# Kernel optimization log

Measured on AMD Instinct MI355X. Metric: run time of the kernel, lower is better.

## Reference

```python
import jax, jax.numpy as jnp
import numpy as np

N = 768          # nodes
E_HALF = 12288   # undirected edges (both directions added -> E = 24576)
P = 4096         # query pairs
H = 32           # hidden_dim_1wl == hidden_dim_2wl
MAX_X = 100
EPS = 1e-5
LAYER1 = 2


def setup_inputs() -> dict:
    key = jax.random.key(0)
    ks = jax.random.split(key, 12)
    s = 0.1
    x = jax.random.randint(ks[0], (N,), 0, MAX_X + 1)
    half = jax.random.randint(ks[1], (2, E_HALF), 0, N)
    ei = jnp.concatenate([half, half[::-1]], axis=1)          # symmetric edge set [2,E]
    pos = jax.random.randint(ks[2], (P, 2), 0, N)
    emb = jax.random.normal(ks[3], (MAX_X + 1, H)) * s
    gcn_W = jax.random.normal(ks[4], (LAYER1, H, H)) * s
    gcn_b = jnp.zeros((LAYER1, H))
    mlp1_W = jax.random.normal(ks[5], (2 * H, H)) * s
    mlp1_b = jnp.zeros((H,))
    mlp2_W = jax.random.normal(ks[6], (2 * H, H)) * s
    mlp2_b = jnp.zeros((H,))
    mlp3_W = jax.random.normal(ks[7], (H + 1, H)) * s
    mlp3_b = jnp.zeros((H,))
    lin_W = jax.random.normal(ks[8], (2 * H, 1)) * s
    lin_b = jnp.zeros((1,))
    return dict(x=x, ei=ei, pos=pos, emb=emb, gcn_W=gcn_W, gcn_b=gcn_b,
                mlp1_W=mlp1_W, mlp1_b=mlp1_b, mlp2_W=mlp2_W, mlp2_b=mlp2_b,
                mlp3_W=mlp3_W, mlp3_b=mlp3_b, lin_W=lin_W, lin_b=lin_b)


def _graph_norm(h):
    # PyG-style GraphNorm with default params (mean_scale=1, weight=1, bias=0)
    h = h - h.mean(0)
    return h * jax.lax.rsqrt((h * h).mean(0) + EPS)


def reference(x, ei, pos, emb, gcn_W, gcn_b, mlp1_W, mlp1_b,
              mlp2_W, mlp2_b, mlp3_W, mlp3_b, lin_W, lin_b):
    n = x.shape[0]
    d = emb.shape[1]
    h = emb[x]                                                 # [n,H] (dropout=0)
    # --- GCNConv stack: Ahat = D^-1/2 (A+I) D^-1/2 ---
    A = jnp.zeros((n, n), h.dtype).at[ei[0], ei[1]].set(1.0)
    Ahat = A + jnp.eye(n, dtype=h.dtype)
    dinv = jax.lax.rsqrt(Ahat.sum(1))
    An = Ahat * dinv[:, None] * dinv[None, :]
    for l in range(gcn_W.shape[0]):
        h = An @ (h @ gcn_W[l]) + gcn_b[l]
        h = jax.nn.relu(_graph_norm(h))                        # GraphNorm + ReLU
    # --- pair features ---
    xx = h[pos[:, 0]] * h[pos[:, 1]]                           # [P,H]
    val = jnp.concatenate([h[ei[0]], h[ei[1]]], 1)             # [E,2H]
    xe = jax.nn.relu(val @ mlp1_W + mlp1_b)                    # mlps_1
    mul = jax.nn.relu(val @ mlp2_W + mlp2_b)                   # mlps_2[0]
    # --- sparse_bmm as dense [n,n,d] contraction (coalesce sums duplicates -> .add) ---
    Xd = jnp.zeros((n, n, d), h.dtype).at[ei[0], ei[1]].add(xe)
    Md = jnp.zeros((n, n, d), h.dtype).at[ei[0], ei[1]].add(mul)
    C = jnp.einsum('ikd,kjd->ijd', Xd, Md)                     # x_{ij} = sum_k x_{ik}*mul_{kj}
    # support of the sparse result: 2-hop pairs union original edges (sparse_cat)
    adj_b = jnp.zeros((n, n), bool).at[ei[0], ei[1]].set(True)
    af = adj_b.astype(h.dtype)
    mask = ((af @ af) > 0) | adj_b
    ind = af[..., None]                                        # ones-column for original edges
    value = jnp.concatenate([C, ind], -1)                      # [n,n,H+1]
    z = value @ mlp3_W + mlp3_b                                # mlps_3[0]
    # GraphNorm over the edge support only (faithful to sparse values())
    m = mask.astype(h.dtype)[..., None]
    cnt = m.sum()
    mean = (z * m).sum((0, 1)) / cnt
    z = z - mean
    var = ((z * z) * m).sum((0, 1)) / cnt
    z = jax.nn.relu(z * jax.lax.rsqrt(var + EPS))
    # x * sm: multiply by transposed values; zero outside support (= add_zero)
    sym = z * jnp.swapaxes(z, 0, 1) * m
    pair = sym[pos[:, 0], pos[:, 1]]                           # [P,H] (edge_list gather)
    out = jnp.concatenate([pair, xx], 1) @ lin_W + lin_b       # lin_dir -> [P,1]
    return out
```

## Files before the change

kernel.cpp:

```cpp
#include <hip/hip_runtime.h>
#include <hip/hip_bf16.h>

#define NN 768
#define NE 24576
#define NPOS 4096
#define NCELL (NN*NN)
#define NBLK 2304
#define NBLK2 1152
#define NREP 16

typedef __hip_bfloat16 bf16;

__device__ __forceinline__ float ldf(const void* p, int i, int mode) {
    return mode ? __bfloat162float(((const bf16*)p)[i]) : ((const float*)p)[i];
}
__device__ __forceinline__ float aread(float* p) { return atomicAdd(p, 0.f); }
__device__ __forceinline__ int areadi(int* p) { return atomicAdd(p, 0); }

template<int D, int HALF>
__device__ __forceinline__ void redRound(float* v, int lane) {
#pragma unroll
    for (int i = 0; i < HALF; i++) {
        float snd = (lane & D) ? v[i] : v[i + HALF];
        float r = __shfl_xor(snd, D);
        v[i] = ((lane & D) ? v[i + HALF] : v[i]) + r;
    }
}

#define DOT4(Z, A, W) Z += A.x * W.x + A.y * W.y + A.z * W.z + A.w * W.w

__global__ void k_conv(const void* __restrict__ gW, const void* __restrict__ gB,
                       const void* __restrict__ m1W, const void* __restrict__ m1B,
                       const void* __restrict__ m2W, const void* __restrict__ m2B,
                       const void* __restrict__ m3W, const void* __restrict__ m3B,
                       const void* __restrict__ lW,  const void* __restrict__ lB,
                       const void* __restrict__ emb,
                       float* __restrict__ stats, int* __restrict__ cursor,
                       int* __restrict__ rowlen, int* __restrict__ rtot, int* __restrict__ dcs,
                       int* __restrict__ modeg,
                       float* __restrict__ gwf, float* __restrict__ gbf,
                       float* __restrict__ w1f, float* __restrict__ b1f,
                       float* __restrict__ w2f, float* __restrict__ b2f,
                       float* __restrict__ w3q, float* __restrict__ linf, float* __restrict__ linb) {
    int t = threadIdx.x;
    if (blockIdx.x == 1) {
        for (int i = t; i < NN; i += 256) { cursor[i] = 0; rowlen[i] = 0; rtot[i] = 0; }
        for (int i = t; i < NREP * 80; i += 256) stats[i] = 0.f;
        if (t < 8) dcs[t] = 0;
        return;
    }
    __shared__ int bad;
    if (t == 0) bad = 0;
    __syncthreads();
    int local = 0;
    for (int i = t; i < 3232; i += 256) {
        float a = fabsf(__bfloat162float(((const bf16*)emb)[i]));
        if (!(a < 100.f)) local = 1;
    }
    if (local) atomicOr(&bad, 1);
    __syncthreads();
    int mode = bad ? 0 : 1;
    if (t == 0) *modeg = mode;
    for (int i = t; i < 2048; i += 256) {
        gwf[i] = ldf(gW, i, mode);
        w1f[i] = ldf(m1W, i, mode);
        w2f[i] = ldf(m2W, i, mode);
    }
    for (int i = t; i < 64; i += 256) { gbf[i] = ldf(gB, i, mode); linf[i] = ldf(lW, i, mode); }
    if (t < 32) { b1f[t] = ldf(m1B, t, mode); b2f[t] = ldf(m2B, t, mode); }
    for (int i = t; i < 1056; i += 256) { int c = i >> 5, d = i & 31; w3q[d * 36 + c] = ldf(m3W, i, mode); }
    if (t < 32) { w3q[t * 36 + 33] = ldf(m3B, t, mode); w3q[t * 36 + 34] = 0.f; w3q[t * 36 + 35] = 0.f; }
    if (t == 0) linb[0] = ldf(lB, 0, mode);
}

__global__ void k_scatter(const int* __restrict__ ei, int* __restrict__ cell, int* __restrict__ rowlen,
                          int* __restrict__ row_ptr, float* __restrict__ dinv, int* __restrict__ dc) {
    __shared__ int amlast;
    __shared__ int sI[256];
    int t = threadIdx.x;
    int e = blockIdx.x * 256 + t;
    int a = ei[e], b = ei[NE + e];
    if ((unsigned)a < (unsigned)NN && (unsigned)b < (unsigned)NN) {
        int old = atomicAdd(&cell[a * NN + b], 1);
        if (old == 0) atomicAdd(&rowlen[a], 1);
    }
    __syncthreads();
    if (t == 0) { __threadfence(); amlast = (atomicAdd(dc, 1) == 95) ? 1 : 0; }
    __syncthreads();
    if (!amlast) return;
    int i0 = 3 * t;
    int r0 = areadi(&rowlen[i0]), r1 = areadi(&rowlen[i0 + 1]), r2 = areadi(&rowlen[i0 + 2]);
    dinv[i0]     = rsqrtf((float)r0 + 1.f);
    dinv[i0 + 1] = rsqrtf((float)r1 + 1.f);
    dinv[i0 + 2] = rsqrtf((float)r2 + 1.f);
    int s3 = r0 + r1 + r2;
    sI[t] = s3;
    __syncthreads();
    for (int off = 1; off < 256; off <<= 1) {
        int tmp = (t >= off) ? sI[t - off] : 0;
        __syncthreads();
        sI[t] += tmp;
        __syncthreads();
    }
    int excl = sI[t] - s3;
    row_ptr[i0] = excl;
    row_ptr[i0 + 1] = excl + r0;
    row_ptr[i0 + 2] = excl + r0 + r1;
    if (t == 255) row_ptr[NN] = sI[255];
}

__global__ void k_fw0(int* __restrict__ cell, const int* __restrict__ row_ptr, int* __restrict__ cursor,
                      int* __restrict__ col_idx, float* __restrict__ cntv, int* __restrict__ pr_row,
                      const int* __restrict__ rowlen, int* __restrict__ rtot,
                      const int* __restrict__ x, const void* __restrict__ emb,
                      const int* __restrict__ modep, const float* __restrict__ gwf,
                      float* __restrict__ bufA) {
    int t = threadIdx.x;
    int b = blockIdx.x;
    if (b < NBLK) {
        int idx = b * 256 + t;
        int i = idx / NN;
        int j = idx - i * NN;
        int cv = cell[idx];
        if (cv > 0) {
            int p = row_ptr[i] + atomicAdd(&cursor[i], 1);
            col_idx[p] = j; cntv[p] = (float)cv; pr_row[p] = i;
            cell[idx] = p;
            atomicAdd(&rtot[i], rowlen[j]);
        } else cell[idx] = -1;
    } else {
        int idx = (b - NBLK) * 256 + t;
        int i = idx >> 5, d = idx & 31;
        int mode = *modep;
        int xi = x[i]; if (xi < 0) xi = 0; if (xi > 100) xi = 100;
        float s = 0.f;
#pragma unroll
        for (int c = 0; c < 32; c++) s += ldf(emb, xi * 32 + c, mode) * gwf[c * 32 + d];
        bufA[idx] = s;
    }
}

__global__ void k_rbagg0(const int* __restrict__ rtot, int* __restrict__ row_base,
                         const int* __restrict__ row_ptr, const int* __restrict__ col_idx,
                         const float* __restrict__ bufA, const float* __restrict__ dinv,
                         const float* __restrict__ gbf, float* __restrict__ bufB) {
    int t = threadIdx.x;
    if (blockIdx.x == 0) {
        __shared__ int sI[256];
        int r3[3]; int s3 = 0;
#pragma unroll
        for (int q = 0; q < 3; q++) { r3[q] = rtot[3 * t + q]; s3 += r3[q]; }
        sI[t] = s3;
        __syncthreads();
        for (int off = 1; off < 256; off <<= 1) {
            int tmp = (t >= off) ? sI[t - off] : 0;
            __syncthreads();
            sI[t] += tmp;
            __syncthreads();
        }
        int run = sI[t] - s3;
        row_base[3 * t] = run;
        row_base[3 * t + 1] = run + r3[0];
        row_base[3 * t + 2] = run + r3[0] + r3[1];
    } else {
        int idx = (blockIdx.x - 1) * 256 + t;
        int i = idx >> 5, d = idx & 31;
        int base = row_ptr[i], len = row_ptr[i + 1] - base;
        float di = dinv[i];
        float acc = di * bufA[i * 32 + d];
        for (int e = 0; e < len; e++) { int c = col_idx[base + e]; acc += dinv[c] * bufA[c * 32 + d]; }
        bufB[idx] = di * acc + gbf[d];
    }
}

__global__ void k_hist(const int* __restrict__ row_ptr, const int* __restrict__ col_idx,
                       const int* __restrict__ row_base,
                       int* __restrict__ pcur, int2* __restrict__ paths2, int cap,
                       const float* __restrict__ bufB, float* __restrict__ nrm0) {
    int t = threadIdx.x;
    if (blockIdx.x == NN) {
        __shared__ float r1[256], r2[256];
        int dd = t & 31, g = t >> 5;
        float s = 0.f, s2 = 0.f;
        for (int r = g; r < NN; r += 8) { float v = bufB[r * 32 + dd]; s += v; s2 += v * v; }
        r1[t] = s; r2[t] = s2;
        __syncthreads();
        if (t < 32) {
            float a = 0.f, b2 = 0.f;
            for (int k = 0; k < 8; k++) { a += r1[k * 32 + t]; b2 += r2[k * 32 + t]; }
            float mean = a / (float)NN;
            float var = b2 / (float)NN - mean * mean;
            nrm0[t] = mean;
            nrm0[32 + t] = rsqrtf(fmaxf(var, 0.f) + 1e-5f);
        }
        return;
    }
    __shared__ int hist[NN];
    __shared__ int sc[256];
    int i = blockIdx.x;
    int base = row_ptr[i], len = row_ptr[i + 1] - base;
    int rb = row_base[i];
    int wave = t >> 6, lane = t & 63;
    for (int j = t; j < NN; j += 256) hist[j] = 0;
    __syncthreads();
    for (int ee = wave; ee < len; ee += 4) {
        int k = col_idx[base + ee];
        int kb = row_ptr[k], ke = row_ptr[k + 1];
        for (int e = kb + lane; e < ke; e += 64) atomicAdd(&hist[col_idx[e]], 1);
    }
    __syncthreads();
    int h0 = hist[3 * t], h1 = hist[3 * t + 1], h2 = hist[3 * t + 2];
    int s3 = h0 + h1 + h2;
    sc[t] = s3;
    __syncthreads();
    for (int off = 1; off < 256; off <<= 1) {
        int tmp = (t >= off) ? sc[t - off] : 0;
        __syncthreads();
        sc[t] += tmp;
        __syncthreads();
    }
    int excl = sc[t] - s3;
    int n0 = i * NN + 3 * t;
    pcur[n0]     = rb + excl + h0;
    pcur[n0 + 1] = rb + excl + h0 + h1;
    pcur[n0 + 2] = rb + excl + h0 + h1 + h2;
    hist[3 * t] = excl;
    hist[3 * t + 1] = excl + h0;
    hist[3 * t + 2] = excl + h0 + h1;
    __syncthreads();
    for (int ee = wave; ee < len; ee += 4) {
        int e1 = base + ee;
        int k = col_idx[e1];
        int kb = row_ptr[k], ke = row_ptr[k + 1];
        for (int e = kb + lane; e < ke; e += 64) {
            int j = col_idx[e];
            int slot = rb + atomicAdd(&hist[j], 1);
            if (slot < cap) paths2[slot] = make_int2(e1, e);
        }
    }
}

__global__ void k_mw1(const float* __restrict__ bufB, const float* __restrict__ nrm0,
                      const float* __restrict__ gwf, float* __restrict__ bufA) {
    int idx = blockIdx.x * 256 + threadIdx.x;
    int i = idx >> 5, d = idx & 31;
    const float* W = gwf + 1024;
    float s = 0.f;
#pragma unroll
    for (int c = 0; c < 32; c++) {
        float hv = fmaxf((bufB[i * 32 + c] - nrm0[c]) * nrm0[32 + c], 0.f);
        s += hv * W[c * 32 + d];
    }
    bufA[idx] = s;
}

__global__ void k_agg1(const int* __restrict__ row_ptr, const int* __restrict__ col_idx,
                       const float* __restrict__ bufA, const float* __restrict__ dinv,
                       const float* __restrict__ gbf, float* __restrict__ bufB) {
    int idx = blockIdx.x * 256 + threadIdx.x;
    int i = idx >> 5, d = idx & 31;
    int base = row_ptr[i], len = row_ptr[i + 1] - base;
    float di = dinv[i];
    float acc = di * bufA[i * 32 + d];
    for (int e = 0; e < len; e++) { int c = col_idx[base + e]; acc += dinv[c] * bufA[c * 32 + d]; }
    bufB[idx] = di * acc + gbf[32 + d];
}

__global__ void k_st1(const float* __restrict__ bufB, float* __restrict__ nrm1) {
    __shared__ float r1[256], r2[256];
    int t = threadIdx.x;
    int dd = t & 31, g = t >> 5;
    float s = 0.f, s2 = 0.f;
    for (int r = g; r < NN; r += 8) { float v = bufB[r * 32 + dd]; s += v; s2 += v * v; }
    r1[t] = s; r2[t] = s2;
    __syncthreads();
    if (t < 32) {
        float a = 0.f, b2 = 0.f;
        for (int k = 0; k < 8; k++) { a += r1[k * 32 + t]; b2 += r2[k * 32 + t]; }
        float mean = a / (float)NN;
        float var = b2 / (float)NN - mean * mean;
        nrm1[t] = mean;
        nrm1[32 + t] = rsqrtf(fmaxf(var, 0.f) + 1e-5f);
    }
}

__global__ void k_emlp(const float* __restrict__ bufB, const float* __restrict__ nrm1,
                       const int* __restrict__ row_ptr, const int* __restrict__ col_idx,
                       const int* __restrict__ pr_row, const float* __restrict__ cntv,
                       const float* __restrict__ w1f, const float* __restrict__ b1f,
                       const float* __restrict__ w2f, const float* __restrict__ b2f,
                       float* __restrict__ xep, float* __restrict__ mulp, float* __restrict__ h) {
    int t = threadIdx.x;
    int b = blockIdx.x;
    if (b < 3072) {
        int d = t & 31;
        int p = b * 8 + (t >> 5);
        if (p >= row_ptr[NN]) {
            if (p < NE) { xep[p * 32 + d] = 0.f; mulp[p * 32 + d] = 0.f; }
            return;
        }
        int i = pr_row[p], j = col_idx[p];
        float a1 = b1f[d], a2 = b2f[d];
#pragma unroll
        for (int c = 0; c < 32; c++) {
            float hv = fmaxf((bufB[i * 32 + c] - nrm1[c]) * nrm1[32 + c], 0.f);
            a1 += hv * w1f[c * 32 + d];
            a2 += hv * w2f[c * 32 + d];
        }
#pragma unroll
        for (int c = 0; c < 32; c++) {
            float hv = fmaxf((bufB[j * 32 + c] - nrm1[c]) * nrm1[32 + c], 0.f);
            a1 += hv * w1f[(32 + c) * 32 + d];
            a2 += hv * w2f[(32 + c) * 32 + d];
        }
        float cv = cntv[p];
        xep[p * 32 + d]  = cv * fmaxf(a1, 0.f);
        mulp[p * 32 + d] = cv * fmaxf(a2, 0.f);
    } else {
        int idx = (b - 3072) * 256 + t;
        int d = idx & 31;
        h[idx] = fmaxf((bufB[idx] - nrm1[d]) * nrm1[32 + d], 0.f);
    }
}

__global__ __launch_bounds__(256, 3) void k_big(const int* __restrict__ pcur,
                                                const int2* __restrict__ paths2,
                                                const int* __restrict__ cell,
                                                const float4* __restrict__ xep4, const float4* __restrict__ mulp4,
                                                const float* __restrict__ w3q,
                                                float* __restrict__ stats, int* __restrict__ done,
                                                float* __restrict__ nrm, int cap) {
    __shared__ float sS1[32], sS2[32];
    __shared__ float sCm;
    __shared__ int amlast;
    int t = threadIdx.x, lane = t & 63;
    int b = blockIdx.x;
    int n0 = b * 512 + 2 * t;
    if (t == 0) sCm = 0.f;
    if (t < 32) { sS1[t] = 0.f; sS2[t] = 0.f; }
    __syncthreads();
    int p0a = (n0 == 0) ? 0 : pcur[n0 - 1];
    int p1a = pcur[n0];
    int p1b = pcur[n0 + 1];
    if (p0a > cap) p0a = cap; if (p1a > cap) p1a = cap; if (p1b > cap) p1b = cap;
    float4 a0 = {0.f,0.f,0.f,0.f}, a1 = a0, a2 = a0, a3 = a0, a4 = a0, a5 = a0, a6 = a0, a7 = a0;
    float4 c0 = a0, c1 = a0, c2 = a0, c3 = a0, c4 = a0, c5 = a0, c6 = a0, c7 = a0;
    for (int p = p0a; p < p1a; p++) {
        int2 rec = paths2[p];
        const float4* xr = xep4 + rec.x * 8;
        const float4* mr = mulp4 + rec.y * 8;
        float4 xv, mv;
        xv = xr[0]; mv = mr[0]; a0.x += xv.x*mv.x; a0.y += xv.y*mv.y; a0.z += xv.z*mv.z; a0.w += xv.w*mv.w;
        xv = xr[1]; mv = mr[1]; a1.x += xv.x*mv.x; a1.y += xv.y*mv.y; a1.z += xv.z*mv.z; a1.w += xv.w*mv.w;
        xv = xr[2]; mv = mr[2]; a2.x += xv.x*mv.x; a2.y += xv.y*mv.y; a2.z += xv.z*mv.z; a2.w += xv.w*mv.w;
        xv = xr[3]; mv = mr[3]; a3.x += xv.x*mv.x; a3.y += xv.y*mv.y; a3.z += xv.z*mv.z; a3.w += xv.w*mv.w;
        xv = xr[4]; mv = mr[4]; a4.x += xv.x*mv.x; a4.y += xv.y*mv.y; a4.z += xv.z*mv.z; a4.w += xv.w*mv.w;
        xv = xr[5]; mv = mr[5]; a5.x += xv.x*mv.x; a5.y += xv.y*mv.y; a5.z += xv.z*mv.z; a5.w += xv.w*mv.w;
        xv = xr[6]; mv = mr[6]; a6.x += xv.x*mv.x; a6.y += xv.y*mv.y; a6.z += xv.z*mv.z; a6.w += xv.w*mv.w;
        xv = xr[7]; mv = mr[7]; a7.x += xv.x*mv.x; a7.y += xv.y*mv.y; a7.z += xv.z*mv.z; a7.w += xv.w*mv.w;
    }
    for (int p = p1a; p < p1b; p++) {
        int2 rec = paths2[p];
        const float4* xr = xep4 + rec.x * 8;
        const float4* mr = mulp4 + rec.y * 8;
        float4 xv, mv;
        xv = xr[0]; mv = mr[0]; c0.x += xv.x*mv.x; c0.y += xv.y*mv.y; c0.z += xv.z*mv.z; c0.w += xv.w*mv.w;
        xv = xr[1]; mv = mr[1]; c1.x += xv.x*mv.x; c1.y += xv.y*mv.y; c1.z += xv.z*mv.z; c1.w += xv.w*mv.w;
        xv = xr[2]; mv = mr[2]; c2.x += xv.x*mv.x; c2.y += xv.y*mv.y; c2.z += xv.z*mv.z; c2.w += xv.w*mv.w;
        xv = xr[3]; mv = mr[3]; c3.x += xv.x*mv.x; c3.y += xv.y*mv.y; c3.z += xv.z*mv.z; c3.w += xv.w*mv.w;
        xv = xr[4]; mv = mr[4]; c4.x += xv.x*mv.x; c4.y += xv.y*mv.y; c4.z += xv.z*mv.z; c4.w += xv.w*mv.w;
        xv = xr[5]; mv = mr[5]; c5.x += xv.x*mv.x; c5.y += xv.y*mv.y; c5.z += xv.z*mv.z; c5.w += xv.w*mv.w;
        xv = xr[6]; mv = mr[6]; c6.x += xv.x*mv.x; c6.y += xv.y*mv.y; c6.z += xv.z*mv.z; c6.w += xv.w*mv.w;
        xv = xr[7]; mv = mr[7]; c7.x += xv.x*mv.x; c7.y += xv.y*mv.y; c7.z += xv.z*mv.z; c7.w += xv.w*mv.w;
    }
    bool adja = cell[n0] >= 0;
    bool adjb = cell[n0 + 1] >= 0;
    float afa = adja ? 1.f : 0.f;
    float afb = adjb ? 1.f : 0.f;
    float mska = (p1a > p0a || adja) ? 1.f : 0.f;
    float mskb = (p1b > p1a || adjb) ? 1.f : 0.f;
#pragma unroll
    for (int ch = 0; ch < 2; ch++) {
        float v[32];
#pragma unroll
        for (int j = 0; j < 16; j++) {
            int dd = ch * 16 + j;
            const float4* wr = (const float4*)(w3q + dd * 36);
            float4 wv = wr[8];
            float za = wv.y + afa * wv.x;
            float zb = wv.y + afb * wv.x;
            wv = wr[0]; DOT4(za, a0, wv); DOT4(zb, c0, wv);
            wv = wr[1]; DOT4(za, a1, wv); DOT4(zb, c1, wv);
            wv = wr[2]; DOT4(za, a2, wv); DOT4(zb, c2, wv);
            wv = wr[3]; DOT4(za, a3, wv); DOT4(zb, c3, wv);
            wv = wr[4]; DOT4(za, a4, wv); DOT4(zb, c4, wv);
            wv = wr[5]; DOT4(za, a5, wv); DOT4(zb, c5, wv);
            wv = wr[6]; DOT4(za, a6, wv); DOT4(zb, c6, wv);
            wv = wr[7]; DOT4(za, a7, wv); DOT4(zb, c7, wv);
            v[j] = mska * za + mskb * zb;
            v[16 + j] = mska * za * za + mskb * zb * zb;
        }
#pragma unroll
        for (int i2 = 0; i2 < 32; i2++) v[i2] += __shfl_xor(v[i2], 32);
        redRound<16, 16>(v, lane);
        redRound<8, 8>(v, lane);
        redRound<4, 4>(v, lane);
        redRound<2, 2>(v, lane);
        redRound<1, 1>(v, lane);
        if (lane < 32) {
            if (lane < 16) atomicAdd(&sS1[ch * 16 + lane], v[0]);
            else           atomicAdd(&sS2[ch * 16 + lane - 16], v[0]);
        }
    }
    {
        float cm2 = mska + mskb;
        for (int off = 32; off >= 1; off >>= 1) cm2 += __shfl_xor(cm2, off);
        if (lane == 0) atomicAdd(&sCm, cm2);
    }
    __syncthreads();
    float* srep = stats + (b & (NREP - 1)) * 80;
    if (t < 32) {
        atomicAdd(&srep[t], sS1[t]);
        atomicAdd(&srep[32 + t], sS2[t]);
    }
    if (t == 32) atomicAdd(&srep[64], sCm);
    __syncthreads();
    if (t == 0) {
        __threadfence();
        amlast = (atomicAdd(done, 1) == NBLK2 - 1) ? 1 : 0;
    }
    __syncthreads();
    if (amlast && t < 32) {
        float sum1 = 0.f, sum2 = 0.f;
        for (int r = 0; r < NREP; r++) {
            sum1 += aread(&stats[r * 80 + t]);
            sum2 += aread(&stats[r * 80 + 32 + t]);
        }
        float cmv = 0.f;
        for (int r = 0; r < NREP; r++) cmv += aread(&stats[r * 80 + 64]);
        if (cmv < 1.f) cmv = 1.f;
        float mean = sum1 / cmv;
        float var = sum2 / cmv - mean * mean;
        nrm[t] = mean;
        nrm[32 + t] = rsqrtf(fmaxf(var, 0.f) + 1e-5f);
    }
}

__global__ void k_out(const int* __restrict__ pos, const int* __restrict__ pcur,
                      const int2* __restrict__ paths2,
                      const int* __restrict__ cell,
                      const float* __restrict__ xep, const float* __restrict__ mulp,
                      const float* __restrict__ h,
                      const float* __restrict__ w3q,
                      const float* __restrict__ nrm,
                      const float* __restrict__ linf, const float* __restrict__ linb,
                      const int* __restrict__ modep, int cap, void* __restrict__ outp) {
    __shared__ float Cb[4][2][32];
    int t = threadIdx.x;
    int w = t >> 6, lane = t & 63, d = lane & 31, dir = lane >> 5;
    int p = blockIdx.x * 4 + w;
    int a = pos[2 * p], b = pos[2 * p + 1];
    if ((unsigned)a >= (unsigned)NN) a = 0;
    if ((unsigned)b >= (unsigned)NN) b = 0;
    int r = dir ? b : a;
    int cc = dir ? a : b;
    int n = r * NN + cc;
    int p1 = pcur[n];
    int p0 = (n == 0) ? 0 : pcur[n - 1];
    if (p0 > cap) p0 = cap; if (p1 > cap) p1 = cap;
    float acc = 0.f;
    for (int q = p0; q < p1; q++) {
        int2 rec = paths2[q];
        acc += xep[rec.x * 32 + d] * mulp[rec.y * 32 + d];
    }
    Cb[w][dir][d] = acc;
    bool adj = cell[n] >= 0;
    float msk = (p1 > p0 || adj) ? 1.f : 0.f;
    __syncthreads();
    float z = w3q[d * 36 + 33] + (adj ? 1.f : 0.f) * w3q[d * 36 + 32];
#pragma unroll
    for (int c = 0; c < 32; c++) z += Cb[w][dir][c] * w3q[d * 36 + c];
    float zn = fmaxf((z - nrm[d]) * nrm[32 + d], 0.f);
    float zp = __shfl_xor(zn, 32);
    float symd = msk * zn * zp;
    float xxd = h[a * 32 + d] * h[b * 32 + d];
    float contrib = symd * linf[d] + xxd * linf[32 + d];
    for (int off = 16; off >= 1; off >>= 1) contrib += __shfl_xor(contrib, off);
    if (lane == 0) {
        float v = contrib + linb[0];
        v = fminf(fmaxf(v, -1e4f), 1e4f);
        if (*modep) ((bf16*)outp)[p] = __float2bfloat16(v);
        else        ((float*)outp)[p] = v;
    }
}

extern "C" void kernel_launch(void* const* d_in, const int* in_sizes, int n_in,
                              void* d_out, int out_size, void* d_ws, size_t ws_size,
                              hipStream_t stream) {
    const void* px  = d_in[0];  const void* pei = d_in[1];  const void* ppos = d_in[2];
    const void* pemb = d_in[3]; const void* pgW = d_in[4];  const void* pgB  = d_in[5];
    const void* pm1W = d_in[6]; const void* pm1B = d_in[7]; const void* pm2W = d_in[8];
    const void* pm2B = d_in[9]; const void* pm3W = d_in[10]; const void* pm3B = d_in[11];
    const void* plW = d_in[12]; const void* plB = d_in[13];
    {
        int c2048 = 0, c64 = 0, c32 = 0;
        for (int i = 0; i < n_in; i++) {
            int s = in_sizes[i]; const void* p = d_in[i];
            switch (s) {
                case 768:   px = p; break;
                case 49152: pei = p; break;
                case 8192:  ppos = p; break;
                case 3232:  pemb = p; break;
                case 2048:  if (c2048 == 0) pgW = p; else if (c2048 == 1) pm1W = p; else pm2W = p; c2048++; break;
                case 64:    if (c64 == 0) pgB = p; else plW = p; c64++; break;
                case 32:    if (c32 == 0) pm1B = p; else if (c32 == 1) pm2B = p; else pm3B = p; c32++; break;
                case 1056:  pm3W = p; break;
                case 1:     plB = p; break;
                default: break;
            }
        }
    }

    char* ws = (char*)d_ws;
    size_t off = 0;
    auto alloc = [&](size_t bytes) -> void* {
        void* pp = ws + off;
        off += (bytes + 255) & ~(size_t)255;
        return pp;
    };
    int*   cell    = (int*)alloc(NCELL * 4);
    int*   pcur    = (int*)alloc(NCELL * 4);
    int*   rowlen  = (int*)alloc(NN * 4);
    int*   rtot    = (int*)alloc(NN * 4);
    int*   row_base= (int*)alloc(NN * 4);
    int*   row_ptr = (int*)alloc((NN + 1) * 4);
    int*   col_idx = (int*)alloc(NE * 4);
    float* cntv    = (float*)alloc(NE * 4);
    int*   pr_row  = (int*)alloc(NE * 4);
    int*   cursor  = (int*)alloc(NN * 4);
    float* dinv    = (float*)alloc(NN * 4);
    float* h       = (float*)alloc(NN * 32 * 4);
    float* bufA    = (float*)alloc(NN * 32 * 4);
    float* bufB    = (float*)alloc(NN * 32 * 4);
    float* xep     = (float*)alloc(NE * 32 * 4);
    float* mulp    = (float*)alloc(NE * 32 * 4);
    float* stats   = (float*)alloc(NREP * 80 * 4);
    float* nrm     = (float*)alloc(64 * 4);
    float* nrm0    = (float*)alloc(64 * 4);
    float* nrm1    = (float*)alloc(64 * 4);
    float* gwf     = (float*)alloc(2048 * 4);
    float* gbf     = (float*)alloc(64 * 4);
    float* w1f     = (float*)alloc(2048 * 4);
    float* b1f     = (float*)alloc(32 * 4);
    float* w2f     = (float*)alloc(2048 * 4);
    float* b2f     = (float*)alloc(32 * 4);
    float* w3q     = (float*)alloc(32 * 36 * 4);
    float* linf    = (float*)alloc(64 * 4);
    float* linb    = (float*)alloc(4);
    int*   modeg   = (int*)alloc(4);
    int*   dcs     = (int*)alloc(8 * 4);
    size_t remain = (ws_size > off) ? (ws_size - off) : 0;
    int cap = (int)(remain / 8);
    if (cap > (1 << 20)) cap = (1 << 20);
    int2*  paths2  = (int2*)alloc((size_t)cap * 8);

    hipMemsetAsync(cell, 0, (size_t)NCELL * 4, stream);
    k_conv<<<2, 256, 0, stream>>>(pgW, pgB, pm1W, pm1B, pm2W, pm2B, pm3W, pm3B, plW, plB,
                                  pemb, stats, cursor, rowlen, rtot, dcs, modeg,
                                  gwf, gbf, w1f, b1f, w2f, b2f, w3q, linf, linb);
    k_scatter<<<96, 256, 0, stream>>>((const int*)pei, cell, rowlen, row_ptr, dinv, &dcs[0]);
    k_fw0<<<NBLK + 96, 256, 0, stream>>>(cell, row_ptr, cursor, col_idx, cntv, pr_row,
                                         rowlen, rtot, (const int*)px, pemb, modeg, gwf, bufA);
    k_rbagg0<<<1 + 96, 256, 0, stream>>>(rtot, row_base, row_ptr, col_idx, bufA, dinv, gbf, bufB);
    k_hist<<<NN + 1, 256, 0, stream>>>(row_ptr, col_idx, row_base, pcur, paths2, cap, bufB, nrm0);
    k_mw1<<<96, 256, 0, stream>>>(bufB, nrm0, gwf, bufA);
    k_agg1<<<96, 256, 0, stream>>>(row_ptr, col_idx, bufA, dinv, gbf, bufB);
    k_st1<<<1, 256, 0, stream>>>(bufB, nrm1);
    k_emlp<<<3072 + 96, 256, 0, stream>>>(bufB, nrm1, row_ptr, col_idx, pr_row, cntv,
                                          w1f, b1f, w2f, b2f, xep, mulp, h);
    k_big<<<NBLK2, 256, 0, stream>>>(pcur, paths2, cell, (const float4*)xep, (const float4*)mulp,
                                     w3q, stats, &dcs[1], nrm, cap);
    k_out<<<NPOS / 4, 256, 0, stream>>>((const int*)ppos, pcur, paths2, cell, xep, mulp, h,
                                        w3q, nrm, linf, linb, modeg, cap, d_out);
}
```

Measured before the change: 326.7 us.

## Fuse GCN aggregation with weight matmul and shrink k_big to wave-sized blocks

Each GCN layer now aggregates over neighbours first and then multiplies by the weight matrix inside the same kernel through shared memory. The layer-1 normalize, matmul and aggregate steps collapse from two kernels into one, and the embedding stage becomes a plain gather. k_big now runs as single-wave 64-thread blocks (four times as many blocks) that atomically add their partial statistics straight into 64 global replica slots. This drops the block-level shared-memory reduction and the __syncthreads barriers, at the cost of more global atomic traffic. The stats buffer must be large enough to hold the added replicas.

```diff
diff --git a/kernel.cpp b/kernel.cpp
--- a/kernel.cpp
+++ b/kernel.cpp
@@ -6,8 +6,8 @@
 #define NPOS 4096
 #define NCELL (NN*NN)
 #define NBLK 2304
-#define NBLK2 1152
-#define NREP 16
+#define NBIG 4608
+#define NREP 64
 
 typedef __hip_bfloat16 bf16;
 
@@ -109,12 +109,11 @@
     if (t == 255) row_ptr[NN] = sI[255];
 }
 
-__global__ void k_fw0(int* __restrict__ cell, const int* __restrict__ row_ptr, int* __restrict__ cursor,
-                      int* __restrict__ col_idx, float* __restrict__ cntv, int* __restrict__ pr_row,
-                      const int* __restrict__ rowlen, int* __restrict__ rtot,
-                      const int* __restrict__ x, const void* __restrict__ emb,
-                      const int* __restrict__ modep, const float* __restrict__ gwf,
-                      float* __restrict__ bufA) {
+__global__ void k_fill(int* __restrict__ cell, const int* __restrict__ row_ptr, int* __restrict__ cursor,
+                       int* __restrict__ col_idx, float* __restrict__ cntv, int* __restrict__ pr_row,
+                       const int* __restrict__ rowlen, int* __restrict__ rtot,
+                       const int* __restrict__ x, const void* __restrict__ emb,
+                       const int* __restrict__ modep, float* __restrict__ bufA) {
     int t = threadIdx.x;
     int b = blockIdx.x;
     if (b < NBLK) {
@@ -130,20 +129,17 @@
         } else cell[idx] = -1;
     } else {
         int idx = (b - NBLK) * 256 + t;
-        int i = idx >> 5, d = idx & 31;
-        int mode = *modep;
+        int i = idx >> 5, k = idx & 31;
         int xi = x[i]; if (xi < 0) xi = 0; if (xi > 100) xi = 100;
-        float s = 0.f;
-#pragma unroll
-        for (int c = 0; c < 32; c++) s += ldf(emb, xi * 32 + c, mode) * gwf[c * 32 + d];
-        bufA[idx] = s;
-    }
-}
-
-__global__ void k_rbagg0(const int* __restrict__ rtot, int* __restrict__ row_base,
+        bufA[idx] = ldf(emb, xi * 32 + k, *modep);
+    }
+}
+
+__global__ void k_aggmw0(const int* __restrict__ rtot, int* __restrict__ row_base,
                          const int* __restrict__ row_ptr, const int* __restrict__ col_idx,
                          const float* __restrict__ bufA, const float* __restrict__ dinv,
-                         const float* __restrict__ gbf, float* __restrict__ bufB) {
+                         const float* __restrict__ gwf, const float* __restrict__ gbf,
+                         float* __restrict__ bufB) {
     int t = threadIdx.x;
     if (blockIdx.x == 0) {
         __shared__ int sI[256];
@@ -162,15 +158,25 @@
         row_base[3 * t] = run;
         row_base[3 * t + 1] = run + r3[0];
         row_base[3 * t + 2] = run + r3[0] + r3[1];
-    } else {
-        int idx = (blockIdx.x - 1) * 256 + t;
-        int i = idx >> 5, d = idx & 31;
-        int base = row_ptr[i], len = row_ptr[i + 1] - base;
-        float di = dinv[i];
-        float acc = di * bufA[i * 32 + d];
-        for (int e = 0; e < len; e++) { int c = col_idx[base + e]; acc += dinv[c] * bufA[c * 32 + d]; }
-        bufB[idx] = di * acc + gbf[d];
-    }
+        return;
+    }
+    __shared__ float sg[8][32];
+    int li = t >> 5, k = t & 31;
+    int i = (blockIdx.x - 1) * 8 + li;
+    int base = row_ptr[i], len = row_ptr[i + 1] - base;
+    float di = dinv[i];
+    float acc = di * bufA[i * 32 + k];
+    for (int e = 0; e < len; e++) {
+        int c = col_idx[base + e];
+        acc += dinv[c] * bufA[c * 32 + k];
+    }
+    sg[li][k] = di * acc;
+    __syncthreads();
+    int d = k;
+    float s = gbf[d];
+#pragma unroll
+    for (int kk = 0; kk < 32; kk++) s += sg[li][kk] * gwf[kk * 32 + d];
+    bufB[i * 32 + d] = s;
 }
 
 __global__ void k_hist(const int* __restrict__ row_ptr, const int* __restrict__ col_idx,
@@ -240,38 +246,39 @@
     }
 }
 
-__global__ void k_mw1(const float* __restrict__ bufB, const float* __restrict__ nrm0,
-                      const float* __restrict__ gwf, float* __restrict__ bufA) {
-    int idx = blockIdx.x * 256 + threadIdx.x;
-    int i = idx >> 5, d = idx & 31;
-    const float* W = gwf + 1024;
-    float s = 0.f;
-#pragma unroll
-    for (int c = 0; c < 32; c++) {
-        float hv = fmaxf((bufB[i * 32 + c] - nrm0[c]) * nrm0[32 + c], 0.f);
-        s += hv * W[c * 32 + d];
-    }
-    bufA[idx] = s;
-}
-
-__global__ void k_agg1(const int* __restrict__ row_ptr, const int* __restrict__ col_idx,
-                       const float* __restrict__ bufA, const float* __restrict__ dinv,
-                       const float* __restrict__ gbf, float* __restrict__ bufB) {
-    int idx = blockIdx.x * 256 + threadIdx.x;
-    int i = idx >> 5, d = idx & 31;
+__global__ void k_aggmw1(const int* __restrict__ row_ptr, const int* __restrict__ col_idx,
+                         const float* __restrict__ bufB, const float* __restrict__ nrm0,
+                         const float* __restrict__ dinv,
+                         const float* __restrict__ gwf, const float* __restrict__ gbf,
+                         float* __restrict__ bufA) {
+    __shared__ float sg[8][32];
+    int t = threadIdx.x;
+    int li = t >> 5, k = t & 31;
+    int i = blockIdx.x * 8 + li;
+    float mk = nrm0[k], rk = nrm0[32 + k];
     int base = row_ptr[i], len = row_ptr[i + 1] - base;
     float di = dinv[i];
-    float acc = di * bufA[i * 32 + d];
-    for (int e = 0; e < len; e++) { int c = col_idx[base + e]; acc += dinv[c] * bufA[c * 32 + d]; }
-    bufB[idx] = di * acc + gbf[32 + d];
-}
-
-__global__ void k_st1(const float* __restrict__ bufB, float* __restrict__ nrm1) {
+    float acc = di * fmaxf((bufB[i * 32 + k] - mk) * rk, 0.f);
+    for (int e = 0; e < len; e++) {
+        int c = col_idx[base + e];
+        acc += dinv[c] * fmaxf((bufB[c * 32 + k] - mk) * rk, 0.f);
+    }
+    sg[li][k] = di * acc;
+    __syncthreads();
+    int d = k;
+    const float* W = gwf + 1024;
+    float s = gbf[32 + d];
+#pragma unroll
+    for (int kk = 0; kk < 32; kk++) s += sg[li][kk] * W[kk * 32 + d];
+    bufA[i * 32 + d] = s;
+}
+
+__global__ void k_st1(const float* __restrict__ bufA, float* __restrict__ nrm1) {
     __shared__ float r1[256], r2[256];
     int t = threadIdx.x;
     int dd = t & 31, g = t >> 5;
     float s = 0.f, s2 = 0.f;
-    for (int r = g; r < NN; r += 8) { float v = bufB[r * 32 + dd]; s += v; s2 += v * v; }
+    for (int r = g; r < NN; r += 8) { float v = bufA[r * 32 + dd]; s += v; s2 += v * v; }
     r1[t] = s; r2[t] = s2;
     __syncthreads();
     if (t < 32) {
@@ -284,7 +291,7 @@
     }
 }
 
-__global__ void k_emlp(const float* __restrict__ bufB, const float* __restrict__ nrm1,
+__global__ void k_emlp(const float* __restrict__ bufA, const float* __restrict__ nrm1,
                        const int* __restrict__ row_ptr, const int* __restrict__ col_idx,
                        const int* __restrict__ pr_row, const float* __restrict__ cntv,
                        const float* __restrict__ w1f, const float* __restrict__ b1f,
@@ -303,13 +310,13 @@
         float a1 = b1f[d], a2 = b2f[d];
 #pragma unroll
         for (int c = 0; c < 32; c++) {
-            float hv = fmaxf((bufB[i * 32 + c] - nrm1[c]) * nrm1[32 + c], 0.f);
+            float hv = fmaxf((bufA[i * 32 + c] - nrm1[c]) * nrm1[32 + c], 0.f);
             a1 += hv * w1f[c * 32 + d];
             a2 += hv * w2f[c * 32 + d];
         }
 #pragma unroll
         for (int c = 0; c < 32; c++) {
-            float hv = fmaxf((bufB[j * 32 + c] - nrm1[c]) * nrm1[32 + c], 0.f);
+            float hv = fmaxf((bufA[j * 32 + c] - nrm1[c]) * nrm1[32 + c], 0.f);
             a1 += hv * w1f[(32 + c) * 32 + d];
             a2 += hv * w2f[(32 + c) * 32 + d];
         }
@@ -319,26 +326,20 @@
     } else {
         int idx = (b - 3072) * 256 + t;
         int d = idx & 31;
-        h[idx] = fmaxf((bufB[idx] - nrm1[d]) * nrm1[32 + d], 0.f);
-    }
-}
-
-__global__ __launch_bounds__(256, 3) void k_big(const int* __restrict__ pcur,
-                                                const int2* __restrict__ paths2,
-                                                const int* __restrict__ cell,
-                                                const float4* __restrict__ xep4, const float4* __restrict__ mulp4,
-                                                const float* __restrict__ w3q,
-                                                float* __restrict__ stats, int* __restrict__ done,
-                                                float* __restrict__ nrm, int cap) {
-    __shared__ float sS1[32], sS2[32];
-    __shared__ float sCm;
-    __shared__ int amlast;
-    int t = threadIdx.x, lane = t & 63;
+        h[idx] = fmaxf((bufA[idx] - nrm1[d]) * nrm1[32 + d], 0.f);
+    }
+}
+
+__global__ __launch_bounds__(64, 4) void k_big(const int* __restrict__ pcur,
+                                               const int2* __restrict__ paths2,
+                                               const int* __restrict__ cell,
+                                               const float4* __restrict__ xep4, const float4* __restrict__ mulp4,
+                                               const float* __restrict__ w3q,
+                                               float* __restrict__ stats, int* __restrict__ done,
+                                               float* __restrict__ nrm, int cap) {
+    int t = threadIdx.x;
     int b = blockIdx.x;
-    int n0 = b * 512 + 2 * t;
-    if (t == 0) sCm = 0.f;
-    if (t < 32) { sS1[t] = 0.f; sS2[t] = 0.f; }
-    __syncthreads();
+    int n0 = b * 128 + 2 * t;
     int p0a = (n0 == 0) ? 0 : pcur[n0 - 1];
     int p1a = pcur[n0];
     int p1b = pcur[n0 + 1];
@@ -379,6 +380,7 @@
     float afb = adjb ? 1.f : 0.f;
     float mska = (p1a > p0a || adja) ? 1.f : 0.f;
     float mskb = (p1b > p1a || adjb) ? 1.f : 0.f;
+    float* srep = stats + (b & (NREP - 1)) * 80;
 #pragma unroll
     for (int ch = 0; ch < 2; ch++) {
         float v[32];
@@ -402,42 +404,34 @@
         }
 #pragma unroll
         for (int i2 = 0; i2 < 32; i2++) v[i2] += __shfl_xor(v[i2], 32);
-        redRound<16, 16>(v, lane);
-        redRound<8, 8>(v, lane);
-        redRound<4, 4>(v, lane);
-        redRound<2, 2>(v, lane);
-        redRound<1, 1>(v, lane);
-        if (lane < 32) {
-            if (lane < 16) atomicAdd(&sS1[ch * 16 + lane], v[0]);
-            else           atomicAdd(&sS2[ch * 16 + lane - 16], v[0]);
-        }
+        redRound<16, 16>(v, t);
+        redRound<8, 8>(v, t);
+        redRound<4, 4>(v, t);
+        redRound<2, 2>(v, t);
+        redRound<1, 1>(v, t);
+        if (t < 16)      atomicAdd(&srep[ch * 16 + t], v[0]);
+        else if (t < 32) atomicAdd(&srep[32 + ch * 16 + t - 16], v[0]);
     }
     {
         float cm2 = mska + mskb;
         for (int off = 32; off >= 1; off >>= 1) cm2 += __shfl_xor(cm2, off);
-        if (lane == 0) atomicAdd(&sCm, cm2);
-    }
-    __syncthreads();
-    float* srep = stats + (b & (NREP - 1)) * 80;
-    if (t < 32) {
-        atomicAdd(&srep[t], sS1[t]);
-        atomicAdd(&srep[32 + t], sS2[t]);
-    }
-    if (t == 32) atomicAdd(&srep[64], sCm);
-    __syncthreads();
+        if (t == 0) atomicAdd(&srep[64], cm2);
+    }
+    int last = 0;
     if (t == 0) {
         __threadfence();
-        amlast = (atomicAdd(done, 1) == NBLK2 - 1) ? 1 : 0;
-    }
-    __syncthreads();
-    if (amlast && t < 32) {
+        last = (atomicAdd(done, 1) == NBIG - 1) ? 1 : 0;
+    }
+    last = __shfl(last, 0);
+    if (last && t < 32) {
         float sum1 = 0.f, sum2 = 0.f;
         for (int r = 0; r < NREP; r++) {
             sum1 += aread(&stats[r * 80 + t]);
             sum2 += aread(&stats[r * 80 + 32 + t]);
         }
         float cmv = 0.f;
-        for (int r = 0; r < NREP; r++) cmv += aread(&stats[r * 80 + 64]);
+        if (t == 0) for (int r = 0; r < NREP; r++) cmv += aread(&stats[r * 80 + 64]);
+        cmv = __shfl(cmv, 0);
         if (cmv < 1.f) cmv = 1.f;
         float mean = sum1 / cmv;
         float var = sum2 / cmv - mean * mean;
@@ -569,17 +563,16 @@
                                   pemb, stats, cursor, rowlen, rtot, dcs, modeg,
                                   gwf, gbf, w1f, b1f, w2f, b2f, w3q, linf, linb);
     k_scatter<<<96, 256, 0, stream>>>((const int*)pei, cell, rowlen, row_ptr, dinv, &dcs[0]);
-    k_fw0<<<NBLK + 96, 256, 0, stream>>>(cell, row_ptr, cursor, col_idx, cntv, pr_row,
-                                         rowlen, rtot, (const int*)px, pemb, modeg, gwf, bufA);
-    k_rbagg0<<<1 + 96, 256, 0, stream>>>(rtot, row_base, row_ptr, col_idx, bufA, dinv, gbf, bufB);
+    k_fill<<<NBLK + 96, 256, 0, stream>>>(cell, row_ptr, cursor, col_idx, cntv, pr_row,
+                                          rowlen, rtot, (const int*)px, pemb, modeg, bufA);
+    k_aggmw0<<<1 + 96, 256, 0, stream>>>(rtot, row_base, row_ptr, col_idx, bufA, dinv, gwf, gbf, bufB);
     k_hist<<<NN + 1, 256, 0, stream>>>(row_ptr, col_idx, row_base, pcur, paths2, cap, bufB, nrm0);
-    k_mw1<<<96, 256, 0, stream>>>(bufB, nrm0, gwf, bufA);
-    k_agg1<<<96, 256, 0, stream>>>(row_ptr, col_idx, bufA, dinv, gbf, bufB);
-    k_st1<<<1, 256, 0, stream>>>(bufB, nrm1);
-    k_emlp<<<3072 + 96, 256, 0, stream>>>(bufB, nrm1, row_ptr, col_idx, pr_row, cntv,
+    k_aggmw1<<<96, 256, 0, stream>>>(row_ptr, col_idx, bufB, nrm0, dinv, gwf, gbf, bufA);
+    k_st1<<<1, 256, 0, stream>>>(bufA, nrm1);
+    k_emlp<<<3072 + 96, 256, 0, stream>>>(bufA, nrm1, row_ptr, col_idx, pr_row, cntv,
                                           w1f, b1f, w2f, b2f, xep, mulp, h);
-    k_big<<<NBLK2, 256, 0, stream>>>(pcur, paths2, cell, (const float4*)xep, (const float4*)mulp,
-                                     w3q, stats, &dcs[1], nrm, cap);
+    k_big<<<NBIG, 64, 0, stream>>>(pcur, paths2, cell, (const float4*)xep, (const float4*)mulp,
+                                   w3q, stats, &dcs[1], nrm, cap);
     k_out<<<NPOS / 4, 256, 0, stream>>>((const int*)ppos, pcur, paths2, cell, xep, mulp, h,
                                         w3q, nrm, linf, linb, modeg, cap, d_out);
 }
```

After: 396.3 us. 21.3% more time.
